# Optimization experiments

Measured on AMD Instinct MI355X. Metric: run time of the kernel, lower is better.

The kernel has to match this reference:

```python
import jax, jax.numpy as jnp
import numpy as np

B, C_L_IN, C_L_OUT, C_J = 512, 64, 64, 16


def setup_inputs() -> dict:
    key = jax.random.key(0)
    ks = jax.random.split(key, 8)
    std = 0.02 / C_L_IN ** 0.5
    return {
        "F_in": jax.random.normal(ks[0], (B, C_L_IN, 4, 4), jnp.float32),
        "theta": jax.random.normal(ks[1], (B, C_J), jnp.float32),
        "W_bias": std * jax.random.normal(ks[2], (C_L_OUT, C_L_IN, 4, 4), jnp.float32),
        "W_cos": std * jax.random.normal(ks[3], (C_L_OUT, C_L_IN, C_J, 4, 4), jnp.float32),
        "W_sin": std * jax.random.normal(ks[4], (C_L_OUT, C_L_IN, C_J, 4, 4), jnp.float32),
        "Wb_bias": std * jax.random.normal(ks[5], (C_L_OUT, C_L_IN, 4, 4), jnp.float32),
        "Wb_cos": std * jax.random.normal(ks[6], (C_L_OUT, C_L_IN, C_J, 4, 4), jnp.float32),
        "Wb_sin": std * jax.random.normal(ks[7], (C_L_OUT, C_L_IN, C_J, 4, 4), jnp.float32),
    }


def reference(F_in, theta, W_bias, W_cos, W_sin, Wb_bias, Wb_cos, Wb_sin):
    cos_t = jnp.cos(theta)  # (B, C_J)
    sin_t = jnp.sin(theta)
    # U, Ub: (B, C_L_out, C_L_in, 4, 4)
    U = (W_bias
         + jnp.einsum('jicpq,bc->bjipq', W_cos, cos_t)
         + jnp.einsum('jicpq,bc->bjipq', W_sin, sin_t))
    Ub = (Wb_bias
          + jnp.einsum('jicpq,bc->bjipq', Wb_cos, cos_t)
          + jnp.einsum('jicpq,bc->bjipq', Wb_sin, sin_t))
    term1 = jnp.einsum('bipq,bjiqr->bjpr', F_in, U)
    term2 = jnp.einsum('bjipq,biqr->bjpr', Ub, F_in)
    return term1 + term2
```

## Files before the change

### kernel.cpp

```cpp
#include <hip/hip_runtime.h>


#define NRO_B   512
#define NRO_CL  64
#define NRO_CJ  16
#define K_DIM   8448
#define M_DIM   2048
#define N_DIM   256
#define SK      8
#define A_ELems ((size_t)M_DIM * K_DIM)
#define B_ELems ((size_t)N_DIM * K_DIM)
#define P_ELems ((size_t)2 * SK * M_DIM * N_DIM)

typedef __attribute__((ext_vector_type(8))) short short8;
typedef __attribute__((ext_vector_type(4))) float floatx4;

__device__ __forceinline__ short f2bf(float x) {
    union { float f; unsigned u; } a; a.f = x;
    unsigned r = a.u + 0x7FFF + ((a.u >> 16) & 1);
    return (short)(r >> 16);
}

__device__ __forceinline__ void load16(const float* p, float w[4][4]) {
    const float4* p4 = (const float4*)p;
    #pragma unroll
    for (int a = 0; a < 4; ++a) {
        float4 x = p4[a];
        w[a][0] = x.x; w[a][1] = x.y; w[a][2] = x.z; w[a][3] = x.w;
    }
}

__global__ __launch_bounds__(256) void nro_prep(
    const float* __restrict__ F_in, const float* __restrict__ theta,
    const float* __restrict__ W_bias, const float* __restrict__ W_cos,
    const float* __restrict__ W_sin,  const float* __restrict__ Wb_bias,
    const float* __restrict__ Wb_cos, const float* __restrict__ Wb_sin,
    short* __restrict__ Abuf,
    short* __restrict__ Bbuf)
{
    if (blockIdx.x < 256) {
        const int unit = blockIdx.x * 4 + (threadIdx.x >> 6);
        const int mat  = unit >> 9;
        const int b    = unit & 511;
        const int i    = threadIdx.x & 63;

        float f[4][4];
        load16(F_in + ((size_t)b * 64 + i) * 16, f);

        float tc[33];
        tc[0] = 1.0f;
        #pragma unroll
        for (int c = 0; c < 16; ++c) {
            float th = theta[b * 16 + c];
            tc[1 + c]  = __cosf(th);
            tc[17 + c] = __sinf(th);
        }

        float rv[4][4];
        #pragma unroll
        for (int a = 0; a < 4; ++a)
            #pragma unroll
            for (int q = 0; q < 4; ++q)
                rv[a][q] = (mat == 0) ? f[a][q] : f[q][a];

        #pragma unroll
        for (int a = 0; a < 4; ++a) {
            short* rowp = Abuf + ((size_t)mat * M_DIM + b * 4 + a) * K_DIM + i * 4;
            #pragma unroll
            for (int cp = 0; cp < 33; ++cp) {
                float t = tc[cp];
                short4 v;
                v.x = f2bf(rv[a][0] * t); v.y = f2bf(rv[a][1] * t);
                v.z = f2bf(rv[a][2] * t); v.w = f2bf(rv[a][3] * t);
                *(short4*)(rowp + cp * 256) = v;
            }
        }
    } else {
        const int unit = (blockIdx.x - 256) * 4 + (threadIdx.x >> 6);
        const int j = unit >> 4;
        const int c = unit & 15;
        const int i = threadIdx.x & 63;

        short* B1 = Bbuf;
        short* B2 = Bbuf + B_ELems;

        const size_t wbase = (((size_t)(j * 64 + i)) * 16 + c) * 16;
        float wc[4][4], ws[4][4], wbc[4][4], wbs[4][4];
        load16(W_cos  + wbase, wc);
        load16(W_sin  + wbase, ws);
        load16(Wb_cos + wbase, wbc);
        load16(Wb_sin + wbase, wbs);

        #pragma unroll
        for (int r = 0; r < 4; ++r) {
            short* n1 = B1 + (size_t)(j * 4 + r) * K_DIM + i * 4;
            short4 v;
            v.x = f2bf(wc[0][r]); v.y = f2bf(wc[1][r]); v.z = f2bf(wc[2][r]); v.w = f2bf(wc[3][r]);
            *(short4*)(n1 + (1 + c) * 256) = v;
            v.x = f2bf(ws[0][r]); v.y = f2bf(ws[1][r]); v.z = f2bf(ws[2][r]); v.w = f2bf(ws[3][r]);
            *(short4*)(n1 + (17 + c) * 256) = v;
        }
        #pragma unroll
        for (int p = 0; p < 4; ++p) {
            short* n2 = B2 + (size_t)(j * 4 + p) * K_DIM + i * 4;
            short4 v;
            v.x = f2bf(wbc[p][0]); v.y = f2bf(wbc[p][1]); v.z = f2bf(wbc[p][2]); v.w = f2bf(wbc[p][3]);
            *(short4*)(n2 + (1 + c) * 256) = v;
            v.x = f2bf(wbs[p][0]); v.y = f2bf(wbs[p][1]); v.z = f2bf(wbs[p][2]); v.w = f2bf(wbs[p][3]);
            *(short4*)(n2 + (17 + c) * 256) = v;
        }

        if (c == 0) {
            float t1[4][4], t2[4][4];
            load16(W_bias  + ((size_t)(j * 64 + i)) * 16, t1);
            load16(Wb_bias + ((size_t)(j * 64 + i)) * 16, t2);
            #pragma unroll
            for (int r = 0; r < 4; ++r) {
                short4 v;
                v.x = f2bf(t1[0][r]); v.y = f2bf(t1[1][r]); v.z = f2bf(t1[2][r]); v.w = f2bf(t1[3][r]);
                *(short4*)(B1 + (size_t)(j * 4 + r) * K_DIM + i * 4) = v;
            }
            #pragma unroll
            for (int p = 0; p < 4; ++p) {
                short4 v;
                v.x = f2bf(t2[p][0]); v.y = f2bf(t2[p][1]); v.z = f2bf(t2[p][2]); v.w = f2bf(t2[p][3]);
                *(short4*)(B2 + (size_t)(j * 4 + p) * K_DIM + i * 4) = v;
            }
        }
    }
}

__global__ __launch_bounds__(256, 2) void nro_gemm(
    const short* __restrict__ Abuf, const short* __restrict__ Bbuf,
    float* __restrict__ part)
{
    const int zs = blockIdx.x;
    const int z  = zs >> 3;
    const int sk = zs & 7;
    const int m0 = blockIdx.y * 64;
    const int kb = sk * (K_DIM / SK);

    const short* A  = Abuf + (size_t)z * A_ELems;
    const short* Bm = Bbuf + (size_t)z * B_ELems;

    __shared__ short As[64 * 32];
    __shared__ short Bs[256 * 32];

    const int tid  = threadIdx.x;
    const int lane = tid & 63;
    const int w    = tid >> 6;
    const int wn   = w * 64;

    floatx4 acc[4][4] = {};

    const int rsub = lane >> 2;
    const int col8 = (lane & 3) * 8;

    for (int kt = 0; kt < 33; ++kt) {
        const int k0 = kb + kt * 32;
        __syncthreads();
        {
            const short* ga = A + (size_t)(m0 + w * 16 + rsub) * K_DIM + k0 + col8;
            __builtin_amdgcn_global_load_lds(
                (const __attribute__((address_space(1))) void*)ga,
                (__attribute__((address_space(3))) void*)(As + (w * 16) * 32),
                16, 0, 0);
        }
        #pragma unroll
        for (int r = 0; r < 4; ++r) {
            const short* gb = Bm + (size_t)(wn + r * 16 + rsub) * K_DIM + k0 + col8;
            __builtin_amdgcn_global_load_lds(
                (const __attribute__((address_space(1))) void*)gb,
                (__attribute__((address_space(3))) void*)(Bs + (wn + r * 16) * 32),
                16, 0, 0);
        }
        __syncthreads();

        const int fr = lane & 15;
        const int fq = (lane >> 4) * 8;
        short8 af[4], bf[4];
        #pragma unroll
        for (int t = 0; t < 4; ++t) {
            af[t] = *(const short8*)(As + (t * 16 + fr) * 32 + fq);
            bf[t] = *(const short8*)(Bs + (wn + t * 16 + fr) * 32 + fq);
        }
        #pragma unroll
        for (int mt = 0; mt < 4; ++mt)
            #pragma unroll
            for (int nt = 0; nt < 4; ++nt)
                acc[mt][nt] = __builtin_amdgcn_mfma_f32_16x16x32_bf16(
                    af[mt], bf[nt], acc[mt][nt], 0, 0, 0);
    }

    const int col  = lane & 15;
    const int row4 = (lane >> 4) * 4;
    #pragma unroll
    for (int mt = 0; mt < 4; ++mt) {
        #pragma unroll
        for (int nt = 0; nt < 4; ++nt) {
            #pragma unroll
            for (int e = 0; e < 4; ++e) {
                const int m = m0 + mt * 16 + row4 + e;
                const int n = wn + nt * 16 + col;
                part[((size_t)zs * M_DIM + m) * N_DIM + n] = acc[mt][nt][e];
            }
        }
    }
}

__global__ __launch_bounds__(256) void nro_reduce(
    const float* __restrict__ part, float* __restrict__ out)
{
    const int t = blockIdx.x * 256 + threadIdx.x;
    const int b = t >> 8;
    const int j = (t >> 2) & 63;
    const int p = t & 3;

    float4 o = make_float4(0.f, 0.f, 0.f, 0.f);
    #pragma unroll
    for (int sk = 0; sk < SK; ++sk) {
        const float4 c1 = *(const float4*)(
            part + ((size_t)sk * M_DIM + b * 4 + p) * N_DIM + j * 4);
        o.x += c1.x; o.y += c1.y; o.z += c1.z; o.w += c1.w;
        const float* p2 = part + ((size_t)(SK + sk) * M_DIM + b * 4) * N_DIM + j * 4 + p;
        o.x += p2[0 * N_DIM]; o.y += p2[1 * N_DIM];
        o.z += p2[2 * N_DIM]; o.w += p2[3 * N_DIM];
    }
    *(float4*)(out + ((size_t)(b * 64 + j) * 16 + p * 4)) = o;
}

__global__ __launch_bounds__(256, 2) void nro_fallback(
    const float* __restrict__ F_in, const float* __restrict__ theta,
    const float* __restrict__ W_bias, const float* __restrict__ W_cos,
    const float* __restrict__ W_sin,  const float* __restrict__ Wb_bias,
    const float* __restrict__ Wb_cos, const float* __restrict__ Wb_sin,
    float* __restrict__ out)
{
    __shared__ float smem[8448];
    const int j      = blockIdx.x >> 3;
    const int isplit = blockIdx.x & 7;
    const int i0     = isplit * 8;
    const int lane   = threadIdx.x & 63;
    const int chunk  = __builtin_amdgcn_readfirstlane(threadIdx.x >> 6);
    const int b      = blockIdx.y * 64 + lane;
    const int tid    = threadIdx.x;
    {
        float4* s4 = (float4*)smem;
        const int base16  = (j * 64 + i0) * 16;
        const int base256 = (j * 64 + i0) * 256;
        if (tid < 32)      s4[tid] = ((const float4*)(W_bias + base16))[tid];
        else if (tid < 64) s4[tid] = ((const float4*)(Wb_bias + base16))[tid - 32];
        #pragma unroll
        for (int r = 0; r < 2; ++r) {
            const int k = r * 256 + tid;
            s4[64 + k]   = ((const float4*)(W_cos  + base256))[k];
            s4[576 + k]  = ((const float4*)(W_sin  + base256))[k];
            s4[1088 + k] = ((const float4*)(Wb_cos + base256))[k];
            s4[1600 + k] = ((const float4*)(Wb_sin + base256))[k];
        }
    }
    float csc[16], css[16];
    #pragma unroll
    for (int c = 0; c < 16; ++c) {
        float t = theta[b * 16 + c];
        csc[c] = __cosf(t); css[c] = __sinf(t);
    }
    __syncthreads();
    float acc[16];
    #pragma unroll
    for (int e = 0; e < 16; ++e) acc[e] = 0.0f;
    #pragma unroll
    for (int ii = 0; ii < 2; ++ii) {
        const int il = chunk * 2 + ii;
        const int i  = i0 + il;
        float f[16];
        const float4* fp = (const float4*)(F_in + (b * 64 + i) * 16);
        #pragma unroll
        for (int v = 0; v < 4; ++v) {
            float4 x = fp[v];
            f[v*4+0]=x.x; f[v*4+1]=x.y; f[v*4+2]=x.z; f[v*4+3]=x.w;
        }
        const float* wb  = smem + il * 16;
        const float* wbb = smem + 128  + il * 16;
        const float* wc  = smem + 256  + il * 256;
        const float* wsn = smem + 2304 + il * 256;
        const float* wbc = smem + 4352 + il * 256;
        const float* wbs = smem + 6400 + il * 256;
        float U[16], Ub[16];
        #pragma unroll
        for (int e = 0; e < 16; ++e) { U[e] = wb[e]; Ub[e] = wbb[e]; }
        #pragma unroll 4
        for (int c = 0; c < 16; ++c) {
            const float cc = csc[c], ss = css[c];
            #pragma unroll
            for (int e = 0; e < 16; ++e) {
                U[e]  = fmaf(wc [c*16+e], cc, U[e]);
                U[e]  = fmaf(wsn[c*16+e], ss, U[e]);
                Ub[e] = fmaf(wbc[c*16+e], cc, Ub[e]);
                Ub[e] = fmaf(wbs[c*16+e], ss, Ub[e]);
            }
        }
        #pragma unroll
        for (int p = 0; p < 4; ++p)
            #pragma unroll
            for (int r = 0; r < 4; ++r) {
                float a = acc[p*4+r];
                #pragma unroll
                for (int q = 0; q < 4; ++q) {
                    a = fmaf(f[p*4+q],  U[q*4+r], a);
                    a = fmaf(Ub[p*4+q], f[q*4+r], a);
                }
                acc[p*4+r] = a;
            }
    }
    __syncthreads();
    if (chunk > 0) {
        float* r = smem + (chunk - 1) * 1088 + lane * 17;
        #pragma unroll
        for (int e = 0; e < 16; ++e) r[e] = acc[e];
    }
    __syncthreads();
    if (chunk == 0) {
        #pragma unroll
        for (int cc = 0; cc < 3; ++cc) {
            const float* r = smem + cc * 1088 + lane * 17;
            #pragma unroll
            for (int e = 0; e < 16; ++e) acc[e] += r[e];
        }
        float* o = out + ((size_t)b * 64 + j) * 16;
        #pragma unroll
        for (int e = 0; e < 16; ++e) atomicAdd(o + e, acc[e]);
    }
}

extern "C" void kernel_launch(void* const* d_in, const int* in_sizes, int n_in,
                              void* d_out, int out_size, void* d_ws, size_t ws_size,
                              hipStream_t stream) {
    const float* F_in    = (const float*)d_in[0];
    const float* theta   = (const float*)d_in[1];
    const float* W_bias  = (const float*)d_in[2];
    const float* W_cos   = (const float*)d_in[3];
    const float* W_sin   = (const float*)d_in[4];
    const float* Wb_bias = (const float*)d_in[5];
    const float* Wb_cos  = (const float*)d_in[6];
    const float* Wb_sin  = (const float*)d_in[7];
    float* out = (float*)d_out;

    const size_t needA = 2 * A_ELems * sizeof(short);
    const size_t needB = 2 * B_ELems * sizeof(short);
    const size_t needP = P_ELems * sizeof(float);
    if (ws_size >= needA + needB + needP) {
        short* Abuf = (short*)d_ws;
        short* Bbuf = (short*)((char*)d_ws + needA);
        float* part = (float*)((char*)d_ws + needA + needB);
        nro_prep<<<512, 256, 0, stream>>>(F_in, theta, W_bias, W_cos, W_sin,
                                          Wb_bias, Wb_cos, Wb_sin, Abuf, Bbuf);
        nro_gemm<<<dim3(16, 32), 256, 0, stream>>>(Abuf, Bbuf, part);
        nro_reduce<<<512, 256, 0, stream>>>(part, out);
    } else {
        hipMemsetAsync(out, 0, (size_t)out_size * sizeof(float), stream);
        dim3 grid(64 * 8, 512 / 64, 1);
        nro_fallback<<<grid, 256, 0, stream>>>(
            F_in, theta, W_bias, W_cos, W_sin, Wb_bias, Wb_cos, Wb_sin, out);
    }
}
```

Before: 124.8 us.

## Build scaled A operand on the fly in GEMM instead of materializing it

The prep kernel no longer writes the large expanded A matrix (F times each cos/sin/1 factor, about 70 MB in bf16). It stores only F and its transpose in fp16, and the GEMM keeps the F tile in LDS and multiplies it by the per-batch trig factor in registers before each MFMA. Operands switch from bf16 to fp16, with f16 MFMA. This removes most of the global write and read traffic for A, at the cost of extra VALU scaling per k-step and fp16 range and precision risk.

```diff
diff --git a/kernel.cpp b/kernel.cpp
--- a/kernel.cpp
+++ b/kernel.cpp
@@ -3,23 +3,17 @@
 
 #define NRO_B   512
 #define NRO_CL  64
-#define NRO_CJ  16
 #define K_DIM   8448
 #define M_DIM   2048
 #define N_DIM   256
 #define SK      8
-#define A_ELems ((size_t)M_DIM * K_DIM)
-#define B_ELems ((size_t)N_DIM * K_DIM)
-#define P_ELems ((size_t)2 * SK * M_DIM * N_DIM)
-
-typedef __attribute__((ext_vector_type(8))) short short8;
+#define B_ELems  ((size_t)N_DIM * K_DIM)
+#define FV_ELems ((size_t)M_DIM * N_DIM)
+#define P_ELems  ((size_t)2 * SK * M_DIM * N_DIM)
+
+typedef __attribute__((ext_vector_type(8))) _Float16 half8;
+typedef __attribute__((ext_vector_type(4))) _Float16 half4_t;
 typedef __attribute__((ext_vector_type(4))) float floatx4;
-
-__device__ __forceinline__ short f2bf(float x) {
-    union { float f; unsigned u; } a; a.f = x;
-    unsigned r = a.u + 0x7FFF + ((a.u >> 16) & 1);
-    return (short)(r >> 16);
-}
 
 __device__ __forceinline__ void load16(const float* p, float w[4][4]) {
     const float4* p4 = (const float4*)p;
@@ -30,182 +24,168 @@
     }
 }
 
+__device__ __forceinline__ half8 scale8(half8 v, _Float16 s) {
+    half8 r;
+    #pragma unroll
+    for (int x = 0; x < 8; ++x) r[x] = v[x] * s;
+    return r;
+}
+
 __global__ __launch_bounds__(256) void nro_prep(
-    const float* __restrict__ F_in, const float* __restrict__ theta,
+    const float* __restrict__ F_in,
     const float* __restrict__ W_bias, const float* __restrict__ W_cos,
     const float* __restrict__ W_sin,  const float* __restrict__ Wb_bias,
     const float* __restrict__ Wb_cos, const float* __restrict__ Wb_sin,
-    short* __restrict__ Abuf,
-    short* __restrict__ Bbuf)
+    _Float16* __restrict__ Bbuf,
+    _Float16* __restrict__ Fv)
 {
-    if (blockIdx.x < 256) {
-        const int unit = blockIdx.x * 4 + (threadIdx.x >> 6);
-        const int mat  = unit >> 9;
-        const int b    = unit & 511;
-        const int i    = threadIdx.x & 63;
-
+    const int w = threadIdx.x >> 6, i = threadIdx.x & 63;
+    if (blockIdx.x < 128) {
+        const int b = blockIdx.x * 4 + w;
         float f[4][4];
         load16(F_in + ((size_t)b * 64 + i) * 16, f);
-
-        float tc[33];
-        tc[0] = 1.0f;
-        #pragma unroll
-        for (int c = 0; c < 16; ++c) {
-            float th = theta[b * 16 + c];
-            tc[1 + c]  = __cosf(th);
-            tc[17 + c] = __sinf(th);
-        }
-
-        float rv[4][4];
-        #pragma unroll
-        for (int a = 0; a < 4; ++a)
-            #pragma unroll
-            for (int q = 0; q < 4; ++q)
-                rv[a][q] = (mat == 0) ? f[a][q] : f[q][a];
-
         #pragma unroll
         for (int a = 0; a < 4; ++a) {
-            short* rowp = Abuf + ((size_t)mat * M_DIM + b * 4 + a) * K_DIM + i * 4;
-            #pragma unroll
-            for (int cp = 0; cp < 33; ++cp) {
-                float t = tc[cp];
-                short4 v;
-                v.x = f2bf(rv[a][0] * t); v.y = f2bf(rv[a][1] * t);
-                v.z = f2bf(rv[a][2] * t); v.w = f2bf(rv[a][3] * t);
-                *(short4*)(rowp + cp * 256) = v;
-            }
+            half4_t v0 = { (_Float16)f[a][0], (_Float16)f[a][1],
+                           (_Float16)f[a][2], (_Float16)f[a][3] };
+            *(half4_t*)(Fv + (size_t)(b * 4 + a) * 256 + i * 4) = v0;
+            half4_t v1 = { (_Float16)f[0][a], (_Float16)f[1][a],
+                           (_Float16)f[2][a], (_Float16)f[3][a] };
+            *(half4_t*)(Fv + FV_ELems + (size_t)(b * 4 + a) * 256 + i * 4) = v1;
         }
     } else {
-        const int unit = (blockIdx.x - 256) * 4 + (threadIdx.x >> 6);
-        const int j = unit >> 4;
-        const int c = unit & 15;
-        const int i = threadIdx.x & 63;
-
-        short* B1 = Bbuf;
-        short* B2 = Bbuf + B_ELems;
-
+        const int unit = (blockIdx.x - 128) * 4 + w;
+        const int j = unit >> 5, c = (unit >> 1) & 15, h = unit & 1;
+        _Float16* Bd = Bbuf + (size_t)h * B_ELems;
         const size_t wbase = (((size_t)(j * 64 + i)) * 16 + c) * 16;
-        float wc[4][4], ws[4][4], wbc[4][4], wbs[4][4];
-        load16(W_cos  + wbase, wc);
-        load16(W_sin  + wbase, ws);
-        load16(Wb_cos + wbase, wbc);
-        load16(Wb_sin + wbase, wbs);
-
-        #pragma unroll
-        for (int r = 0; r < 4; ++r) {
-            short* n1 = B1 + (size_t)(j * 4 + r) * K_DIM + i * 4;
-            short4 v;
-            v.x = f2bf(wc[0][r]); v.y = f2bf(wc[1][r]); v.z = f2bf(wc[2][r]); v.w = f2bf(wc[3][r]);
-            *(short4*)(n1 + (1 + c) * 256) = v;
-            v.x = f2bf(ws[0][r]); v.y = f2bf(ws[1][r]); v.z = f2bf(ws[2][r]); v.w = f2bf(ws[3][r]);
-            *(short4*)(n1 + (17 + c) * 256) = v;
-        }
-        #pragma unroll
-        for (int p = 0; p < 4; ++p) {
-            short* n2 = B2 + (size_t)(j * 4 + p) * K_DIM + i * 4;
-            short4 v;
-            v.x = f2bf(wbc[p][0]); v.y = f2bf(wbc[p][1]); v.z = f2bf(wbc[p][2]); v.w = f2bf(wbc[p][3]);
-            *(short4*)(n2 + (1 + c) * 256) = v;
-            v.x = f2bf(wbs[p][0]); v.y = f2bf(wbs[p][1]); v.z = f2bf(wbs[p][2]); v.w = f2bf(wbs[p][3]);
-            *(short4*)(n2 + (17 + c) * 256) = v;
-        }
-
+
+        float wc4[4][4], ws4[4][4];
+        if (h == 0) { load16(W_cos  + wbase, wc4); load16(W_sin  + wbase, ws4); }
+        else        { load16(Wb_cos + wbase, wc4); load16(Wb_sin + wbase, ws4); }
+
+        #pragma unroll
+        for (int a = 0; a < 4; ++a) {
+            _Float16* n = Bd + (size_t)(j * 4 + a) * K_DIM + i * 4;
+            half4_t vc, vs;
+            if (h == 0) {
+                vc = (half4_t){ (_Float16)wc4[0][a], (_Float16)wc4[1][a],
+                                (_Float16)wc4[2][a], (_Float16)wc4[3][a] };
+                vs = (half4_t){ (_Float16)ws4[0][a], (_Float16)ws4[1][a],
+                                (_Float16)ws4[2][a], (_Float16)ws4[3][a] };
+            } else {
+                vc = (half4_t){ (_Float16)wc4[a][0], (_Float16)wc4[a][1],
+                                (_Float16)wc4[a][2], (_Float16)wc4[a][3] };
+                vs = (half4_t){ (_Float16)ws4[a][0], (_Float16)ws4[a][1],
+                                (_Float16)ws4[a][2], (_Float16)ws4[a][3] };
+            }
+            *(half4_t*)(n + (1 + c)  * 256) = vc;
+            *(half4_t*)(n + (17 + c) * 256) = vs;
+        }
         if (c == 0) {
-            float t1[4][4], t2[4][4];
-            load16(W_bias  + ((size_t)(j * 64 + i)) * 16, t1);
-            load16(Wb_bias + ((size_t)(j * 64 + i)) * 16, t2);
-            #pragma unroll
-            for (int r = 0; r < 4; ++r) {
-                short4 v;
-                v.x = f2bf(t1[0][r]); v.y = f2bf(t1[1][r]); v.z = f2bf(t1[2][r]); v.w = f2bf(t1[3][r]);
-                *(short4*)(B1 + (size_t)(j * 4 + r) * K_DIM + i * 4) = v;
-            }
-            #pragma unroll
-            for (int p = 0; p < 4; ++p) {
-                short4 v;
-                v.x = f2bf(t2[p][0]); v.y = f2bf(t2[p][1]); v.z = f2bf(t2[p][2]); v.w = f2bf(t2[p][3]);
-                *(short4*)(B2 + (size_t)(j * 4 + p) * K_DIM + i * 4) = v;
+            float t[4][4];
+            load16(((h == 0) ? W_bias : Wb_bias) + ((size_t)(j * 64 + i)) * 16, t);
+            #pragma unroll
+            for (int a = 0; a < 4; ++a) {
+                half4_t v;
+                if (h == 0) v = (half4_t){ (_Float16)t[0][a], (_Float16)t[1][a],
+                                           (_Float16)t[2][a], (_Float16)t[3][a] };
+                else        v = (half4_t){ (_Float16)t[a][0], (_Float16)t[a][1],
+                                           (_Float16)t[a][2], (_Float16)t[a][3] };
+                *(half4_t*)(Bd + (size_t)(j * 4 + a) * K_DIM + i * 4) = v;
             }
         }
     }
 }
 
 __global__ __launch_bounds__(256, 2) void nro_gemm(
-    const short* __restrict__ Abuf, const short* __restrict__ Bbuf,
+    const _Float16* __restrict__ Bbuf, const _Float16* __restrict__ Fv,
+    const float* __restrict__ theta,
     float* __restrict__ part)
 {
     const int zs = blockIdx.x;
     const int z  = zs >> 3;
     const int sk = zs & 7;
     const int m0 = blockIdx.y * 64;
-    const int kb = sk * (K_DIM / SK);
-
-    const short* A  = Abuf + (size_t)z * A_ELems;
-    const short* Bm = Bbuf + (size_t)z * B_ELems;
-
-    __shared__ short As[64 * 32];
-    __shared__ short Bs[256 * 32];
+
+    const _Float16* Bm = Bbuf + (size_t)z * B_ELems;
+    const _Float16* Fm = Fv + (size_t)z * FV_ELems + (size_t)m0 * 256;
+
+    __shared__ _Float16 Fs[64 * 264];
+    __shared__ _Float16 Bs[256 * 32];
+    __shared__ float    trig[16 * 34];
 
     const int tid  = threadIdx.x;
     const int lane = tid & 63;
     const int w    = tid >> 6;
     const int wn   = w * 64;
 
+    #pragma unroll
+    for (int kk = 0; kk < 8; ++kk) {
+        const int idx = kk * 256 + tid;
+        const int row = idx >> 5, cf = idx & 31;
+        half8 v = *(const half8*)(Fm + (size_t)row * 256 + cf * 8);
+        *(half8*)(Fs + row * 264 + cf * 8) = v;
+    }
+    {
+        const int bl = tid >> 4, c = tid & 15;
+        const float th = theta[(m0 >> 2) * 16 + tid];
+        trig[bl * 34 + 1 + c]  = __cosf(th);
+        trig[bl * 34 + 17 + c] = __sinf(th);
+        if (c == 0) trig[bl * 34] = 1.0f;
+    }
+
     floatx4 acc[4][4] = {};
-
-    const int rsub = lane >> 2;
-    const int col8 = (lane & 3) * 8;
+    const int rsub = lane >> 2, col8 = (lane & 3) * 8;
+    const int fr = lane & 15,  fq = (lane >> 4) * 8;
+    _Float16 tv[4] = {};
 
     for (int kt = 0; kt < 33; ++kt) {
-        const int k0 = kb + kt * 32;
+        const int g   = sk * 33 + kt;
+        const int cp  = g >> 3;
+        const int iq0 = (g & 7) * 32;
+        const int k0  = g * 32;
         __syncthreads();
-        {
-            const short* ga = A + (size_t)(m0 + w * 16 + rsub) * K_DIM + k0 + col8;
-            __builtin_amdgcn_global_load_lds(
-                (const __attribute__((address_space(1))) void*)ga,
-                (__attribute__((address_space(3))) void*)(As + (w * 16) * 32),
-                16, 0, 0);
-        }
         #pragma unroll
         for (int r = 0; r < 4; ++r) {
-            const short* gb = Bm + (size_t)(wn + r * 16 + rsub) * K_DIM + k0 + col8;
+            const _Float16* gb = Bm + (size_t)(wn + r * 16 + rsub) * K_DIM + k0 + col8;
             __builtin_amdgcn_global_load_lds(
                 (const __attribute__((address_space(1))) void*)gb,
                 (__attribute__((address_space(3))) void*)(Bs + (wn + r * 16) * 32),
                 16, 0, 0);
         }
+        if (kt == 0 || (g & 7) == 0) {
+            #pragma unroll
+            for (int t = 0; t < 4; ++t)
+                tv[t] = (_Float16)trig[(t * 4 + (fr >> 2)) * 34 + cp];
+        }
         __syncthreads();
 
-        const int fr = lane & 15;
-        const int fq = (lane >> 4) * 8;
-        short8 af[4], bf[4];
+        half8 af[4], bf[4];
         #pragma unroll
         for (int t = 0; t < 4; ++t) {
-            af[t] = *(const short8*)(As + (t * 16 + fr) * 32 + fq);
-            bf[t] = *(const short8*)(Bs + (wn + t * 16 + fr) * 32 + fq);
+            half8 fvf = *(const half8*)(Fs + (t * 16 + fr) * 264 + iq0 + fq);
+            af[t] = scale8(fvf, tv[t]);
+            bf[t] = *(const half8*)(Bs + (wn + t * 16 + fr) * 32 + fq);
         }
         #pragma unroll
         for (int mt = 0; mt < 4; ++mt)
             #pragma unroll
             for (int nt = 0; nt < 4; ++nt)
-                acc[mt][nt] = __builtin_amdgcn_mfma_f32_16x16x32_bf16(
+                acc[mt][nt] = __builtin_amdgcn_mfma_f32_16x16x32_f16(
                     af[mt], bf[nt], acc[mt][nt], 0, 0, 0);
     }
 
-    const int col  = lane & 15;
-    const int row4 = (lane >> 4) * 4;
-    #pragma unroll
-    for (int mt = 0; mt < 4; ++mt) {
-        #pragma unroll
-        for (int nt = 0; nt < 4; ++nt) {
+    const int col = lane & 15, row4 = (lane >> 4) * 4;
+    #pragma unroll
+    for (int mt = 0; mt < 4; ++mt)
+        #pragma unroll
+        for (int nt = 0; nt < 4; ++nt)
             #pragma unroll
             for (int e = 0; e < 4; ++e) {
                 const int m = m0 + mt * 16 + row4 + e;
                 const int n = wn + nt * 16 + col;
                 part[((size_t)zs * M_DIM + m) * N_DIM + n] = acc[mt][nt][e];
             }
-        }
-    }
 }
 
 __global__ __launch_bounds__(256) void nro_reduce(
@@ -346,16 +326,16 @@
     const float* Wb_sin  = (const float*)d_in[7];
     float* out = (float*)d_out;
 
-    const size_t needA = 2 * A_ELems * sizeof(short);
-    const size_t needB = 2 * B_ELems * sizeof(short);
-    const size_t needP = P_ELems * sizeof(float);
-    if (ws_size >= needA + needB + needP) {
-        short* Abuf = (short*)d_ws;
-        short* Bbuf = (short*)((char*)d_ws + needA);
-        float* part = (float*)((char*)d_ws + needA + needB);
-        nro_prep<<<512, 256, 0, stream>>>(F_in, theta, W_bias, W_cos, W_sin,
-                                          Wb_bias, Wb_cos, Wb_sin, Abuf, Bbuf);
-        nro_gemm<<<dim3(16, 32), 256, 0, stream>>>(Abuf, Bbuf, part);
+    const size_t needB  = 2 * B_ELems  * sizeof(_Float16);
+    const size_t needFv = 2 * FV_ELems * sizeof(_Float16);
+    const size_t needP  = P_ELems * sizeof(float);
+    if (ws_size >= needB + needFv + needP) {
+        _Float16* Bbuf = (_Float16*)d_ws;
+        _Float16* Fv   = (_Float16*)((char*)d_ws + needB);
+        float*    part = (float*)((char*)d_ws + needB + needFv);
+        nro_prep<<<640, 256, 0, stream>>>(F_in, W_bias, W_cos, W_sin,
+                                          Wb_bias, Wb_cos, Wb_sin, Bbuf, Fv);
+        nro_gemm<<<dim3(16, 32), 256, 0, stream>>>(Bbuf, Fv, theta, part);
         nro_reduce<<<512, 256, 0, stream>>>(part, out);
     } else {
         hipMemsetAsync(out, 0, (size_t)out_size * sizeof(float), stream);
```

Result: faster. 115.0 us (-7.8%).
